# Optimization experiments

Measured on AMD Instinct MI355X. Metric: run time of the kernel, lower is better.

The kernel has to match this reference:

```python
import jax, jax.numpy as jnp
import numpy as np

EMBED_DIM = 768
NUM_HEADS = 12
HEAD_DIM = EMBED_DIM // NUM_HEADS
SEGMENT_LENGTHS = [2048, 4096, 8192]
DILATION_RATES = [1, 2, 4]
SCALE = 1.0 / np.sqrt(HEAD_DIM)
B, S = 1, 8192


def setup_inputs() -> dict:
    key = jax.random.key(0)
    ks = jax.random.split(key, 5)
    std = 1.0 / np.sqrt(EMBED_DIM)
    return {
        "x": jax.random.normal(ks[0], (B, S, EMBED_DIM), dtype=jnp.float32),
        "Wqkv": jax.random.normal(ks[1], (EMBED_DIM, 3 * EMBED_DIM), dtype=jnp.float32) * std,
        "bqkv": jax.random.normal(ks[2], (3 * EMBED_DIM,), dtype=jnp.float32) * 0.01,
        "Wout": jax.random.normal(ks[3], (EMBED_DIM, EMBED_DIM), dtype=jnp.float32) * std,
        "bout": jax.random.normal(ks[4], (EMBED_DIM,), dtype=jnp.float32) * 0.01,
    }


def _attend(q, k, v):
    # q,k,v: [B,H,L,D]; full softmax attention (non-causal)
    scores = jnp.einsum("bhqd,bhkd->bhqk", q, k) * SCALE
    w = jax.nn.softmax(scores, axis=-1)
    return jnp.einsum("bhqk,bhkd->bhqd", w, v)


def reference(x, Wqkv, bqkv, Wout, bout):
    b, s, _ = x.shape
    qkv = x @ Wqkv + bqkv                                  # [B,S,3E]
    qkv = qkv.reshape(b, s, 3, NUM_HEADS, HEAD_DIM)
    qkv = jnp.transpose(qkv, (2, 0, 3, 1, 4))              # [3,B,H,S,D]
    q, k, v = qkv[0], qkv[1], qkv[2]

    outputs = []
    for seg_len, dil in zip(SEGMENT_LENGTHS, DILATION_RATES):
        if seg_len > s:
            continue
        if dil > 1:
            idx = np.arange(0, s, dil)[:seg_len]           # static indices
            seg_out = _attend(q[:, :, idx, :], k[:, :, idx, :], v[:, :, idx, :])
            full = jnp.zeros((b, NUM_HEADS, s, HEAD_DIM), dtype=seg_out.dtype)
            full = full.at[:, :, idx, :].set(seg_out)
        else:
            seg_out = _attend(q[:, :, :seg_len, :], k[:, :, :seg_len, :], v[:, :, :seg_len, :])
            pad = s - seg_out.shape[2]
            full = jnp.pad(seg_out, ((0, 0), (0, 0), (0, pad), (0, 0))) if pad > 0 else seg_out
        outputs.append(full)

    out = jnp.mean(jnp.stack(outputs), axis=0) if len(outputs) > 1 else outputs[0]
    out = jnp.transpose(out, (0, 2, 1, 3)).reshape(b, s, EMBED_DIM)
    return out @ Wout + bout
```

## Files before the change

kernel.cpp:

```cpp
#include <hip/hip_runtime.h>
#include <hip/hip_bf16.h>

typedef float f32x4 __attribute__((ext_vector_type(4)));
typedef float fvec4 __attribute__((ext_vector_type(4)));
typedef __bf16 bf16x8 __attribute__((ext_vector_type(8)));

__device__ inline float fexp2(float x) {
#if __has_builtin(__builtin_amdgcn_exp2f)
    return __builtin_amdgcn_exp2f(x);
#else
    return exp2f(x);
#endif
}

#define MFMA_BF16(a, b, c) __builtin_amdgcn_mfma_f32_16x16x32_bf16((a), (b), (c), 0, 0, 0)

__device__ __forceinline__ void gl2lds16(const void* g, void* l) {
    __builtin_amdgcn_global_load_lds((const __attribute__((address_space(1))) void*)g,
                                     (__attribute__((address_space(3))) void*)l, 16, 0, 0);
}

#define SEG1OFF ((size_t)12 * 2048 * 64)
#define SEG2OFF ((size_t)12 * 6144 * 64)
#define QSCALE 0.18033688f

__global__ __launch_bounds__(256) void cvt_kernel(const float* __restrict__ in,
                                                  __bf16* __restrict__ out, int n8) {
    int i = blockIdx.x * 256 + threadIdx.x;
    if (i >= n8) return;
    fvec4 a = ((const fvec4*)in)[2 * i];
    fvec4 b = ((const fvec4*)in)[2 * i + 1];
    bf16x8 o;
    o[0] = (__bf16)a[0]; o[1] = (__bf16)a[1]; o[2] = (__bf16)a[2]; o[3] = (__bf16)a[3];
    o[4] = (__bf16)b[0]; o[5] = (__bf16)b[1]; o[6] = (__bf16)b[2]; o[7] = (__bf16)b[3];
    ((bf16x8*)out)[i] = o;
}

__global__ __launch_bounds__(256) void transpose_cvt_kernel(const float* __restrict__ src,
                                                            __bf16* __restrict__ dst, int N) {
    int n = blockIdx.x * 256 + threadIdx.x;
    int kg = blockIdx.y;
    if (n >= N) return;
    bf16x8 o;
#pragma unroll
    for (int j = 0; j < 8; j++) o[j] = (__bf16)src[(size_t)(kg * 8 + j) * N + n];
    *(bf16x8*)&dst[(size_t)n * 768 + kg * 8] = o;
}

__global__ __launch_bounds__(256) void vtrans_kernel(const __bf16* __restrict__ Vc,
                                                     __bf16* __restrict__ Vt) {
    __shared__ __bf16 T[64][68];
    int bid = blockIdx.x;
    int Lc, head, t;
    size_t soff;
    if (bid < 768)       { Lc = 4096; head = bid >> 6; t = bid & 63; soff = SEG1OFF; }
    else if (bid < 1152) { int i = bid - 768; Lc = 2048; head = i >> 5; t = i & 31; soff = 0; }
    else                 { int i = bid - 1152; Lc = 2048; head = i >> 5; t = i & 31; soff = SEG2OFF; }
    const __bf16* src = Vc + soff + (size_t)head * Lc * 64;
    __bf16* dst = Vt + soff + (size_t)head * 64 * Lc;
    int tid = threadIdx.x;
#pragma unroll
    for (int it = 0; it < 2; it++) {
        int s = tid + it * 256;
        int kvr = s >> 3, d8 = (s & 7) * 8;
        bf16x8 vv = *(const bf16x8*)&src[(size_t)(t * 64 + kvr) * 64 + d8];
#pragma unroll
        for (int j = 0; j < 8; j++) T[d8 + j][kvr] = vv[j];
    }
    __syncthreads();
#pragma unroll
    for (int it = 0; it < 2; it++) {
        int s = tid + it * 256;
        int d = s >> 3, ck = s & 7;
        int kb = (ck >> 2) * 32 + (ck & 3) * 4;
        bf16x8 o;
#pragma unroll
        for (int J = 0; J < 8; J++) o[J] = T[d][kb + (J & 3) + (J >> 2) * 16];
        *(bf16x8*)&dst[(size_t)d * Lc + t * 64 + ck * 8] = o;
    }
}

__global__ __launch_bounds__(256, 2) void gemm_kernel(
    const __bf16* __restrict__ Ab, const __bf16* __restrict__ Bt,
    const float* __restrict__ bias,
    __bf16* __restrict__ Qc, __bf16* __restrict__ Kc, __bf16* __restrict__ Vc,
    float* __restrict__ Co, int mode) {
    __shared__ __align__(16) char smem[34816];
    __bf16* Al = (__bf16*)smem;
    __bf16* Bl = Al + 128 * 64;
    __bf16* T  = (__bf16*)smem;
    int tid = threadIdx.x;
    int wave = tid >> 6, lane = tid & 63;
    int quad = lane >> 4, l15 = lane & 15;
    int bm = blockIdx.x * 128, bn = blockIdx.y * 128;
    int wm = (wave >> 1) * 64, wn = (wave & 1) * 64;
    int swzA = tid & 7;
    f32x4 acc[4][4] = {};
    for (int k0 = 0; k0 < 768; k0 += 64) {
        __syncthreads();
#pragma unroll
        for (int j = 0; j < 4; j++) {
            int s = j * 256 + tid;
            int row = s >> 3;
            int ch = swzA ^ (row & 7);
            gl2lds16(&Ab[(size_t)(bm + row) * 768 + k0 + ch * 8],
                     (char*)smem + j * 4096 + wave * 1024);
            gl2lds16(&Bt[(size_t)(bn + row) * 768 + k0 + ch * 8],
                     (char*)smem + 16384 + j * 4096 + wave * 1024);
        }
        __syncthreads();
#pragma unroll
        for (int ks = 0; ks < 2; ks++) {
            bf16x8 af[4], bfr[4];
#pragma unroll
            for (int i = 0; i < 4; i++) {
                int row = wm + i * 16 + l15;
                af[i] = *(const bf16x8*)&Al[row * 64 + (((ks * 4 + quad) ^ (row & 7)) * 8)];
            }
#pragma unroll
            for (int j = 0; j < 4; j++) {
                int row = wn + j * 16 + l15;
                bfr[j] = *(const bf16x8*)&Bl[row * 64 + (((ks * 4 + quad) ^ (row & 7)) * 8)];
            }
#pragma unroll
            for (int i = 0; i < 4; i++)
#pragma unroll
                for (int j = 0; j < 4; j++)
                    acc[i][j] = MFMA_BF16(af[i], bfr[j], acc[i][j]);
        }
    }
    if (mode == 0) {
        int which = blockIdx.y / 6;
        int h0 = (blockIdx.y % 6) * 2;
        float scl = which == 0 ? QSCALE : 1.0f;
        float bv[4];
#pragma unroll
        for (int j = 0; j < 4; j++) bv[j] = bias[bn + wn + j * 16 + l15];
        __syncthreads();
#pragma unroll
        for (int i = 0; i < 4; i++)
#pragma unroll
            for (int j = 0; j < 4; j++) {
                int col = wn + j * 16 + l15;
#pragma unroll
                for (int r = 0; r < 4; r++) {
                    int row = wm + i * 16 + quad * 4 + r;
                    int ch = ((col >> 3) & 8) | (((col >> 3) & 7) ^ (row & 7));
                    T[row * 136 + ch * 8 + (col & 7)] =
                        (__bf16)((acc[i][j][r] + bv[j]) * scl);
                }
            }
        __syncthreads();
        __bf16* dst = which == 0 ? Qc : (which == 1 ? Kc : Vc);
        int rr = tid >> 4;
        int c8 = tid & 15;
        int hh = c8 >> 3, d8 = c8 & 7;
        int h = h0 + hh;
        __bf16* p0 = dst + ((size_t)h * 2048 * 64) + d8 * 8;
        __bf16* p1 = dst + SEG1OFF + ((size_t)h * 4096 * 64) + d8 * 8;
        __bf16* p2 = dst + SEG2OFF + ((size_t)h * 2048 * 64) + d8 * 8;
#pragma unroll
        for (int pass = 0; pass < 8; pass++) {
            int row = pass * 16 + rr;
            int pos = bm + row;
            int ch = (c8 & 8) | ((c8 & 7) ^ (row & 7));
            bf16x8 v = *(const bf16x8*)&T[row * 136 + ch * 8];
            if (pos < 2048) *(bf16x8*)&p0[(size_t)pos * 64] = v;
            if (!(pos & 1)) *(bf16x8*)&p1[(size_t)(pos >> 1) * 64] = v;
            if (!(pos & 3)) *(bf16x8*)&p2[(size_t)(pos >> 2) * 64] = v;
        }
    } else {
        int quad4 = quad * 4;
#pragma unroll
        for (int j = 0; j < 4; j++) {
            int c = bn + wn + j * 16 + l15;
            float bv = bias[c];
#pragma unroll
            for (int i = 0; i < 4; i++)
#pragma unroll
                for (int r = 0; r < 4; r++) {
                    int row = bm + wm + i * 16 + quad4 + r;
                    Co[(size_t)row * 768 + c] = acc[i][j][r] + bv;
                }
        }
    }
}

__global__ __launch_bounds__(256, 2) void attn_kernel(
    const __bf16* __restrict__ Qcb, const __bf16* __restrict__ Kcb,
    const __bf16* __restrict__ Vtb,
    float* __restrict__ O0, float* __restrict__ O1a, float* __restrict__ O1b,
    float* __restrict__ O2, float* __restrict__ L0, float* __restrict__ L1a,
    float* __restrict__ L1b, float* __restrict__ L2) {
    __shared__ __bf16 Kl[64 * 64];
    __shared__ __bf16 Vl[64 * 64];
    int bid = blockIdx.x;
    int seg, half = 0, head, qt, Lc;
    if (bid < 768)      { int i = bid >> 1; half = bid & 1; head = i >> 5; qt = i & 31; Lc = 4096; seg = 1; }
    else if (bid < 960) { int i = bid - 768; head = i >> 4; qt = i & 15; Lc = 2048; seg = 0; }
    else                { int i = bid - 960; head = i >> 4; qt = i & 15; Lc = 2048; seg = 2; }
    size_t soff = seg == 0 ? 0 : (seg == 1 ? SEG1OFF : SEG2OFF);
    const __bf16* Qh = Qcb + soff + (size_t)head * Lc * 64;
    const __bf16* Kh = Kcb + soff + (size_t)head * Lc * 64;
    const __bf16* Vh = Vtb + soff + (size_t)head * 64 * Lc;
    float* Ob;
    float* Lb;
    if (seg == 0)      { Ob = O0; Lb = L0 + head * 2048; }
    else if (seg == 1) { Ob = half ? O1b : O1a; Lb = (half ? L1b : L1a) + head * 4096; }
    else               { Ob = O2; Lb = L2 + head * 2048; }
    int kvb = (seg == 1) ? half * 32 : 0;
    int tid = threadIdx.x, wave = tid >> 6, lane = tid & 63;
    int quad = lane >> 4, l15 = lane & 15;
    bf16x8 qf[2][2];
#pragma unroll
    for (int qg = 0; qg < 2; qg++) {
        size_t qpos = (size_t)(qt * 128 + wave * 32 + qg * 16 + l15);
        qf[qg][0] = *(const bf16x8*)&Qh[qpos * 64 + quad * 8];
        qf[qg][1] = *(const bf16x8*)&Qh[qpos * 64 + 32 + quad * 8];
    }
    f32x4 o[2][4] = {};
    float lrun[2] = {0.f, 0.f};
    int kv0 = tid >> 3, cl0 = tid & 7;
    int kdb0 = cl0 ^ (kv0 & 7);
    int kv1 = kv0 + 32, kdb1 = cl0 ^ (kv1 & 7);
    char* KlB = (char*)Kl;
    char* VlB = (char*)Vl;
    int swz = l15 & 7;
    for (int nt = 0; nt < 32; nt++) {
        int t0 = (kvb + nt) * 64;
        __syncthreads();
        gl2lds16(&Kh[(size_t)(t0 + kv0) * 64 + kdb0 * 8], KlB + wave * 1024);
        gl2lds16(&Kh[(size_t)(t0 + kv1) * 64 + kdb1 * 8], KlB + 4096 + wave * 1024);
        gl2lds16(&Vh[(size_t)kv0 * Lc + t0 + kdb0 * 8], VlB + wave * 1024);
        gl2lds16(&Vh[(size_t)kv1 * Lc + t0 + kdb1 * 8], VlB + 4096 + wave * 1024);
        __syncthreads();
        f32x4 sarr[4][2];
#pragma unroll
        for (int c = 0; c < 4; c++) {
            int krow = (c * 16 + l15) * 64;
            bf16x8 kf0 = *(const bf16x8*)&Kl[krow + ((quad ^ swz) * 8)];
            bf16x8 kf1 = *(const bf16x8*)&Kl[krow + (((4 + quad) ^ swz) * 8)];
#pragma unroll
            for (int qg = 0; qg < 2; qg++) {
                f32x4 z = {};
                z = MFMA_BF16(kf0, qf[qg][0], z);
                sarr[c][qg] = MFMA_BF16(kf1, qf[qg][1], z);
            }
        }
        bf16x8 pf8[2][2];
#pragma unroll
        for (int qg = 0; qg < 2; qg++)
#pragma unroll
            for (int c = 0; c < 4; c++)
#pragma unroll
                for (int r = 0; r < 4; r++) {
                    float p = fexp2(sarr[c][qg][r]);
                    lrun[qg] += p;
                    pf8[qg][c >> 1][(c & 1) * 4 + r] = (__bf16)p;
                }
#pragma unroll
        for (int u = 0; u < 2; u++)
#pragma unroll
            for (int ds = 0; ds < 4; ds++) {
                int d = ds * 16 + l15;
                bf16x8 vf = *(const bf16x8*)&Vl[d * 64 + (((u * 4 + quad) ^ swz) * 8)];
                o[0][ds] = MFMA_BF16(vf, pf8[0][u], o[0][ds]);
                o[1][ds] = MFMA_BF16(vf, pf8[1][u], o[1][ds]);
            }
    }
#pragma unroll
    for (int qg = 0; qg < 2; qg++) {
        float l = lrun[qg];
        l += __shfl_xor(l, 16, 64);
        l += __shfl_xor(l, 32, 64);
        int pos = qt * 128 + wave * 32 + qg * 16 + l15;
        float* orow = Ob + (size_t)pos * 768 + head * 64;
#pragma unroll
        for (int ds = 0; ds < 4; ds++)
            *(f32x4*)&orow[ds * 16 + quad * 4] = o[qg][ds];
        if (lane < 16) Lb[qt * 128 + wave * 32 + qg * 16 + lane] = l;
    }
}

__global__ __launch_bounds__(256) void combine_kernel(
    const float* __restrict__ O0, const float* __restrict__ O1a,
    const float* __restrict__ O1b, const float* __restrict__ O2,
    const float* __restrict__ L0, const float* __restrict__ L1a,
    const float* __restrict__ L1b, const float* __restrict__ L2,
    __bf16* __restrict__ attnF) {
    int g = blockIdx.x * 256 + threadIdx.x;
    int q = g / 96;
    int cs = (g - q * 96) * 8;
    int head = cs >> 6;
    f32x4 a0 = {}, a1 = {};
    if (q < 2048) {
        float inv = 1.0f / L0[head * 2048 + q];
        const f32x4* p = (const f32x4*)&O0[(size_t)q * 768 + cs];
        a0 += p[0] * inv; a1 += p[1] * inv;
    }
    if (!(q & 1)) {
        int p1 = q >> 1;
        float inv = 1.0f / (L1a[head * 4096 + p1] + L1b[head * 4096 + p1]);
        const f32x4* pa = (const f32x4*)&O1a[(size_t)p1 * 768 + cs];
        const f32x4* pb = (const f32x4*)&O1b[(size_t)p1 * 768 + cs];
        a0 += (pa[0] + pb[0]) * inv; a1 += (pa[1] + pb[1]) * inv;
    }
    if (!(q & 3)) {
        int p2 = q >> 2;
        float inv = 1.0f / L2[head * 2048 + p2];
        const f32x4* p = (const f32x4*)&O2[(size_t)p2 * 768 + cs];
        a0 += p[0] * inv; a1 += p[1] * inv;
    }
    const float third = 1.0f / 3.0f;
    bf16x8 ov;
    ov[0] = (__bf16)(a0[0] * third); ov[1] = (__bf16)(a0[1] * third);
    ov[2] = (__bf16)(a0[2] * third); ov[3] = (__bf16)(a0[3] * third);
    ov[4] = (__bf16)(a1[0] * third); ov[5] = (__bf16)(a1[1] * third);
    ov[6] = (__bf16)(a1[2] * third); ov[7] = (__bf16)(a1[3] * third);
    *(bf16x8*)&attnF[(size_t)q * 768 + cs] = ov;
}

extern "C" void kernel_launch(void* const* d_in, const int* in_sizes, int n_in,
                              void* d_out, int out_size, void* d_ws, size_t ws_size,
                              hipStream_t stream) {
    const float* x    = (const float*)d_in[0];
    const float* Wqkv = (const float*)d_in[1];
    const float* bqkv = (const float*)d_in[2];
    const float* Wout = (const float*)d_in[3];
    const float* bout = (const float*)d_in[4];
    float* out = (float*)d_out;
    (void)in_sizes; (void)n_in; (void)out_size; (void)ws_size;

    char* ws = (char*)d_ws;
    size_t off = 0;
    auto take = [&](size_t bytes) -> void* {
        void* p = ws + off;
        off += (bytes + 255) & ~(size_t)255;
        return p;
    };
    const size_t QKV_ELEMS = (size_t)12 * 8192 * 64;
    __bf16* xb    = (__bf16*)take((size_t)8192 * 768 * 2);
    __bf16* WqkvT = (__bf16*)take((size_t)2304 * 768 * 2);
    __bf16* WoutT = (__bf16*)take((size_t)768 * 768 * 2);
    __bf16* Qc    = (__bf16*)take(QKV_ELEMS * 2);
    __bf16* Kc    = (__bf16*)take(QKV_ELEMS * 2);
    __bf16* Vc    = (__bf16*)take(QKV_ELEMS * 2);
    __bf16* Vt    = (__bf16*)take(QKV_ELEMS * 2);
    float*  O0    = (float*)take((size_t)2048 * 768 * 4);
    float*  O1a   = (float*)take((size_t)4096 * 768 * 4);
    float*  O1b   = (float*)take((size_t)4096 * 768 * 4);
    float*  O2    = (float*)take((size_t)2048 * 768 * 4);
    float*  L0    = (float*)take((size_t)12 * 2048 * 4);
    float*  L1a   = (float*)take((size_t)12 * 4096 * 4);
    float*  L1b   = (float*)take((size_t)12 * 4096 * 4);
    float*  L2    = (float*)take((size_t)12 * 2048 * 4);
    __bf16* attnF = Qc;

    cvt_kernel<<<3072, 256, 0, stream>>>(x, xb, 8192 * 768 / 8);
    transpose_cvt_kernel<<<dim3(9, 96), 256, 0, stream>>>(Wqkv, WqkvT, 2304);
    transpose_cvt_kernel<<<dim3(3, 96), 256, 0, stream>>>(Wout, WoutT, 768);
    gemm_kernel<<<dim3(64, 18), 256, 0, stream>>>(xb, WqkvT, bqkv, Qc, Kc, Vc,
                                                  nullptr, 0);
    vtrans_kernel<<<1536, 256, 0, stream>>>(Vc, Vt);
    attn_kernel<<<1152, 256, 0, stream>>>(Qc, Kc, Vt, O0, O1a, O1b, O2, L0, L1a, L1b, L2);
    combine_kernel<<<3072, 256, 0, stream>>>(O0, O1a, O1b, O2, L0, L1a, L1b, L2, attnF);
    gemm_kernel<<<dim3(64, 6), 256, 0, stream>>>(attnF, WoutT, bout, nullptr, nullptr,
                                                 nullptr, out, 1);
}
```

Measured before the change: 259.7 us.

## Split long-segment attention KV into four pieces and retile output GEMM

The 4096-length segment's attention is now split four ways along the KV axis instead of two. Each block runs 16 KV tiles, the launch grows to 1920 blocks, and the combine kernel sums four partial outputs and row sums. The output projection gets its own kernel with 64-row tiles, giving 768 blocks instead of 384 so the GPU is filled better. The probability packing uses the packed bf16 convert builtin, and some partial buffers reuse dead workspace (xb, Vc). The trade-off is extra partial-output traffic and a heavier combine kernel.

```diff
diff --git a/kernel.cpp b/kernel.cpp
--- a/kernel.cpp
+++ b/kernel.cpp
@@ -4,12 +4,22 @@
 typedef float f32x4 __attribute__((ext_vector_type(4)));
 typedef float fvec4 __attribute__((ext_vector_type(4)));
 typedef __bf16 bf16x8 __attribute__((ext_vector_type(8)));
+typedef __bf16 bf16x2 __attribute__((ext_vector_type(2)));
 
 __device__ inline float fexp2(float x) {
 #if __has_builtin(__builtin_amdgcn_exp2f)
     return __builtin_amdgcn_exp2f(x);
 #else
     return exp2f(x);
+#endif
+}
+
+__device__ __forceinline__ bf16x2 pk_bf16(float a, float b) {
+#if __has_builtin(__builtin_amdgcn_cvt_pk_bf16_f32)
+    auto t = __builtin_amdgcn_cvt_pk_bf16_f32(a, b);
+    return __builtin_bit_cast(bf16x2, t);
+#else
+    bf16x2 r; r[0] = (__bf16)a; r[1] = (__bf16)b; return r;
 #endif
 }
 
@@ -80,11 +90,10 @@
     }
 }
 
-__global__ __launch_bounds__(256, 2) void gemm_kernel(
+__global__ __launch_bounds__(256, 2) void gemm_qkv_kernel(
     const __bf16* __restrict__ Ab, const __bf16* __restrict__ Bt,
     const float* __restrict__ bias,
-    __bf16* __restrict__ Qc, __bf16* __restrict__ Kc, __bf16* __restrict__ Vc,
-    float* __restrict__ Co, int mode) {
+    __bf16* __restrict__ Qc, __bf16* __restrict__ Kc, __bf16* __restrict__ Vc) {
     __shared__ __align__(16) char smem[34816];
     __bf16* Al = (__bf16*)smem;
     __bf16* Bl = Al + 128 * 64;
@@ -129,60 +138,109 @@
                     acc[i][j] = MFMA_BF16(af[i], bfr[j], acc[i][j]);
         }
     }
-    if (mode == 0) {
-        int which = blockIdx.y / 6;
-        int h0 = (blockIdx.y % 6) * 2;
-        float scl = which == 0 ? QSCALE : 1.0f;
-        float bv[4];
-#pragma unroll
-        for (int j = 0; j < 4; j++) bv[j] = bias[bn + wn + j * 16 + l15];
-        __syncthreads();
+    int which = blockIdx.y / 6;
+    int h0 = (blockIdx.y % 6) * 2;
+    float scl = which == 0 ? QSCALE : 1.0f;
+    float bv[4];
+#pragma unroll
+    for (int j = 0; j < 4; j++) bv[j] = bias[bn + wn + j * 16 + l15];
+    __syncthreads();
+#pragma unroll
+    for (int i = 0; i < 4; i++)
+#pragma unroll
+        for (int j = 0; j < 4; j++) {
+            int col = wn + j * 16 + l15;
+#pragma unroll
+            for (int r = 0; r < 4; r++) {
+                int row = wm + i * 16 + quad * 4 + r;
+                int ch = ((col >> 3) & 8) | (((col >> 3) & 7) ^ (row & 7));
+                T[row * 136 + ch * 8 + (col & 7)] =
+                    (__bf16)((acc[i][j][r] + bv[j]) * scl);
+            }
+        }
+    __syncthreads();
+    __bf16* dst = which == 0 ? Qc : (which == 1 ? Kc : Vc);
+    int rr = tid >> 4;
+    int c8 = tid & 15;
+    int hh = c8 >> 3, d8 = c8 & 7;
+    int h = h0 + hh;
+    __bf16* p0 = dst + ((size_t)h * 2048 * 64) + d8 * 8;
+    __bf16* p1 = dst + SEG1OFF + ((size_t)h * 4096 * 64) + d8 * 8;
+    __bf16* p2 = dst + SEG2OFF + ((size_t)h * 2048 * 64) + d8 * 8;
+#pragma unroll
+    for (int pass = 0; pass < 8; pass++) {
+        int row = pass * 16 + rr;
+        int pos = bm + row;
+        int ch = (c8 & 8) | ((c8 & 7) ^ (row & 7));
+        bf16x8 v = *(const bf16x8*)&T[row * 136 + ch * 8];
+        if (pos < 2048) *(bf16x8*)&p0[(size_t)pos * 64] = v;
+        if (!(pos & 1)) *(bf16x8*)&p1[(size_t)(pos >> 1) * 64] = v;
+        if (!(pos & 3)) *(bf16x8*)&p2[(size_t)(pos >> 2) * 64] = v;
+    }
+}
+
+__global__ __launch_bounds__(256) void gemm_out_kernel(
+    const __bf16* __restrict__ Ab, const __bf16* __restrict__ Bt,
+    const float* __restrict__ bias, float* __restrict__ Co) {
+    __shared__ __align__(16) char smem[24576];
+    __bf16* Al = (__bf16*)smem;
+    __bf16* Bl = Al + 64 * 64;
+    int tid = threadIdx.x;
+    int wave = tid >> 6, lane = tid & 63;
+    int quad = lane >> 4, l15 = lane & 15;
+    int bm = blockIdx.x * 64, bn = blockIdx.y * 128;
+    int wn = wave * 32;
+    f32x4 acc[4][2] = {};
+    for (int k0 = 0; k0 < 768; k0 += 64) {
+        __syncthreads();
+#pragma unroll
+        for (int j = 0; j < 2; j++) {
+            int s = j * 256 + tid;
+            int row = s >> 3;
+            int ch = (s & 7) ^ (row & 7);
+            gl2lds16(&Ab[(size_t)(bm + row) * 768 + k0 + ch * 8],
+                     (char*)smem + j * 4096 + wave * 1024);
+        }
+#pragma unroll
+        for (int j = 0; j < 4; j++) {
+            int s = j * 256 + tid;
+            int row = s >> 3;
+            int ch = (s & 7) ^ (row & 7);
+            gl2lds16(&Bt[(size_t)(bn + row) * 768 + k0 + ch * 8],
+                     (char*)smem + 8192 + j * 4096 + wave * 1024);
+        }
+        __syncthreads();
+#pragma unroll
+        for (int ks = 0; ks < 2; ks++) {
+            bf16x8 af[4], bfr[2];
+#pragma unroll
+            for (int i = 0; i < 4; i++) {
+                int row = i * 16 + l15;
+                af[i] = *(const bf16x8*)&Al[row * 64 + (((ks * 4 + quad) ^ (row & 7)) * 8)];
+            }
+#pragma unroll
+            for (int j = 0; j < 2; j++) {
+                int row = wn + j * 16 + l15;
+                bfr[j] = *(const bf16x8*)&Bl[row * 64 + (((ks * 4 + quad) ^ (row & 7)) * 8)];
+            }
+#pragma unroll
+            for (int i = 0; i < 4; i++)
+#pragma unroll
+                for (int j = 0; j < 2; j++)
+                    acc[i][j] = MFMA_BF16(af[i], bfr[j], acc[i][j]);
+        }
+    }
+#pragma unroll
+    for (int j = 0; j < 2; j++) {
+        int c = bn + wn + j * 16 + l15;
+        float bv = bias[c];
 #pragma unroll
         for (int i = 0; i < 4; i++)
 #pragma unroll
-            for (int j = 0; j < 4; j++) {
-                int col = wn + j * 16 + l15;
-#pragma unroll
-                for (int r = 0; r < 4; r++) {
-                    int row = wm + i * 16 + quad * 4 + r;
-                    int ch = ((col >> 3) & 8) | (((col >> 3) & 7) ^ (row & 7));
-                    T[row * 136 + ch * 8 + (col & 7)] =
-                        (__bf16)((acc[i][j][r] + bv[j]) * scl);
-                }
-            }
-        __syncthreads();
-        __bf16* dst = which == 0 ? Qc : (which == 1 ? Kc : Vc);
-        int rr = tid >> 4;
-        int c8 = tid & 15;
-        int hh = c8 >> 3, d8 = c8 & 7;
-        int h = h0 + hh;
-        __bf16* p0 = dst + ((size_t)h * 2048 * 64) + d8 * 8;
-        __bf16* p1 = dst + SEG1OFF + ((size_t)h * 4096 * 64) + d8 * 8;
-        __bf16* p2 = dst + SEG2OFF + ((size_t)h * 2048 * 64) + d8 * 8;
-#pragma unroll
-        for (int pass = 0; pass < 8; pass++) {
-            int row = pass * 16 + rr;
-            int pos = bm + row;
-            int ch = (c8 & 8) | ((c8 & 7) ^ (row & 7));
-            bf16x8 v = *(const bf16x8*)&T[row * 136 + ch * 8];
-            if (pos < 2048) *(bf16x8*)&p0[(size_t)pos * 64] = v;
-            if (!(pos & 1)) *(bf16x8*)&p1[(size_t)(pos >> 1) * 64] = v;
-            if (!(pos & 3)) *(bf16x8*)&p2[(size_t)(pos >> 2) * 64] = v;
-        }
-    } else {
-        int quad4 = quad * 4;
-#pragma unroll
-        for (int j = 0; j < 4; j++) {
-            int c = bn + wn + j * 16 + l15;
-            float bv = bias[c];
-#pragma unroll
-            for (int i = 0; i < 4; i++)
-#pragma unroll
-                for (int r = 0; r < 4; r++) {
-                    int row = bm + wm + i * 16 + quad4 + r;
-                    Co[(size_t)row * 768 + c] = acc[i][j][r] + bv;
-                }
-        }
+            for (int r = 0; r < 4; r++) {
+                int row = bm + i * 16 + quad * 4 + r;
+                Co[(size_t)row * 768 + c] = acc[i][j][r] + bv;
+            }
     }
 }
 
@@ -190,15 +248,17 @@
     const __bf16* __restrict__ Qcb, const __bf16* __restrict__ Kcb,
     const __bf16* __restrict__ Vtb,
     float* __restrict__ O0, float* __restrict__ O1a, float* __restrict__ O1b,
-    float* __restrict__ O2, float* __restrict__ L0, float* __restrict__ L1a,
-    float* __restrict__ L1b, float* __restrict__ L2) {
+    float* __restrict__ O1c, float* __restrict__ O1d, float* __restrict__ O2,
+    float* __restrict__ L0, float* __restrict__ L1a, float* __restrict__ L1b,
+    float* __restrict__ L1c, float* __restrict__ L1d, float* __restrict__ L2) {
     __shared__ __bf16 Kl[64 * 64];
     __shared__ __bf16 Vl[64 * 64];
     int bid = blockIdx.x;
-    int seg, half = 0, head, qt, Lc;
-    if (bid < 768)      { int i = bid >> 1; half = bid & 1; head = i >> 5; qt = i & 31; Lc = 4096; seg = 1; }
-    else if (bid < 960) { int i = bid - 768; head = i >> 4; qt = i & 15; Lc = 2048; seg = 0; }
-    else                { int i = bid - 960; head = i >> 4; qt = i & 15; Lc = 2048; seg = 2; }
+    int seg, piece = 0, head, qt, Lc, iters;
+    if (bid < 192)      { seg = 0; head = bid >> 4; qt = bid & 15; Lc = 2048; iters = 32; }
+    else if (bid < 384) { int i = bid - 192; seg = 2; head = i >> 4; qt = i & 15; Lc = 2048; iters = 32; }
+    else                { int i = bid - 384; seg = 1; head = i >> 7; int r = i & 127;
+                          qt = r >> 2; piece = r & 3; Lc = 4096; iters = 16; }
     size_t soff = seg == 0 ? 0 : (seg == 1 ? SEG1OFF : SEG2OFF);
     const __bf16* Qh = Qcb + soff + (size_t)head * Lc * 64;
     const __bf16* Kh = Kcb + soff + (size_t)head * Lc * 64;
@@ -206,9 +266,12 @@
     float* Ob;
     float* Lb;
     if (seg == 0)      { Ob = O0; Lb = L0 + head * 2048; }
-    else if (seg == 1) { Ob = half ? O1b : O1a; Lb = (half ? L1b : L1a) + head * 4096; }
-    else               { Ob = O2; Lb = L2 + head * 2048; }
-    int kvb = (seg == 1) ? half * 32 : 0;
+    else if (seg == 2) { Ob = O2; Lb = L2 + head * 2048; }
+    else {
+        Ob = piece == 0 ? O1a : (piece == 1 ? O1b : (piece == 2 ? O1c : O1d));
+        Lb = (piece == 0 ? L1a : (piece == 1 ? L1b : (piece == 2 ? L1c : L1d))) + head * 4096;
+    }
+    int kvb = piece * 16;
     int tid = threadIdx.x, wave = tid >> 6, lane = tid & 63;
     int quad = lane >> 4, l15 = lane & 15;
     bf16x8 qf[2][2];
@@ -226,7 +289,7 @@
     char* KlB = (char*)Kl;
     char* VlB = (char*)Vl;
     int swz = l15 & 7;
-    for (int nt = 0; nt < 32; nt++) {
+    for (int nt = 0; nt < iters; nt++) {
         int t0 = (kvb + nt) * 64;
         __syncthreads();
         gl2lds16(&Kh[(size_t)(t0 + kv0) * 64 + kdb0 * 8], KlB + wave * 1024);
@@ -247,25 +310,27 @@
                 sarr[c][qg] = MFMA_BF16(kf1, qf[qg][1], z);
             }
         }
-        bf16x8 pf8[2][2];
+        union { bf16x8 v8; bf16x2 v2[4]; } pf8[2][2];
 #pragma unroll
         for (int qg = 0; qg < 2; qg++)
 #pragma unroll
-            for (int c = 0; c < 4; c++)
-#pragma unroll
-                for (int r = 0; r < 4; r++) {
-                    float p = fexp2(sarr[c][qg][r]);
-                    lrun[qg] += p;
-                    pf8[qg][c >> 1][(c & 1) * 4 + r] = (__bf16)p;
-                }
+            for (int c = 0; c < 4; c++) {
+                float p0 = fexp2(sarr[c][qg][0]);
+                float p1 = fexp2(sarr[c][qg][1]);
+                float p2 = fexp2(sarr[c][qg][2]);
+                float p3 = fexp2(sarr[c][qg][3]);
+                lrun[qg] += (p0 + p1) + (p2 + p3);
+                pf8[qg][c >> 1].v2[(c & 1) * 2 + 0] = pk_bf16(p0, p1);
+                pf8[qg][c >> 1].v2[(c & 1) * 2 + 1] = pk_bf16(p2, p3);
+            }
 #pragma unroll
         for (int u = 0; u < 2; u++)
 #pragma unroll
             for (int ds = 0; ds < 4; ds++) {
                 int d = ds * 16 + l15;
                 bf16x8 vf = *(const bf16x8*)&Vl[d * 64 + (((u * 4 + quad) ^ swz) * 8)];
-                o[0][ds] = MFMA_BF16(vf, pf8[0][u], o[0][ds]);
-                o[1][ds] = MFMA_BF16(vf, pf8[1][u], o[1][ds]);
+                o[0][ds] = MFMA_BF16(vf, pf8[0][u].v8, o[0][ds]);
+                o[1][ds] = MFMA_BF16(vf, pf8[1][u].v8, o[1][ds]);
             }
     }
 #pragma unroll
@@ -284,9 +349,11 @@
 
 __global__ __launch_bounds__(256) void combine_kernel(
     const float* __restrict__ O0, const float* __restrict__ O1a,
-    const float* __restrict__ O1b, const float* __restrict__ O2,
+    const float* __restrict__ O1b, const float* __restrict__ O1c,
+    const float* __restrict__ O1d, const float* __restrict__ O2,
     const float* __restrict__ L0, const float* __restrict__ L1a,
-    const float* __restrict__ L1b, const float* __restrict__ L2,
+    const float* __restrict__ L1b, const float* __restrict__ L1c,
+    const float* __restrict__ L1d, const float* __restrict__ L2,
     __bf16* __restrict__ attnF) {
     int g = blockIdx.x * 256 + threadIdx.x;
     int q = g / 96;
@@ -300,10 +367,15 @@
     }
     if (!(q & 1)) {
         int p1 = q >> 1;
-        float inv = 1.0f / (L1a[head * 4096 + p1] + L1b[head * 4096 + p1]);
-        const f32x4* pa = (const f32x4*)&O1a[(size_t)p1 * 768 + cs];
-        const f32x4* pb = (const f32x4*)&O1b[(size_t)p1 * 768 + cs];
-        a0 += (pa[0] + pb[0]) * inv; a1 += (pa[1] + pb[1]) * inv;
+        int li = head * 4096 + p1;
+        float inv = 1.0f / (L1a[li] + L1b[li] + L1c[li] + L1d[li]);
+        size_t ro = (size_t)p1 * 768 + cs;
+        const f32x4* pa = (const f32x4*)&O1a[ro];
+        const f32x4* pb = (const f32x4*)&O1b[ro];
+        const f32x4* pc = (const f32x4*)&O1c[ro];
+        const f32x4* pd = (const f32x4*)&O1d[ro];
+        a0 += ((pa[0] + pb[0]) + (pc[0] + pd[0])) * inv;
+        a1 += ((pa[1] + pb[1]) + (pc[1] + pd[1])) * inv;
     }
     if (!(q & 3)) {
         int p2 = q >> 2;
@@ -346,24 +418,28 @@
     __bf16* Kc    = (__bf16*)take(QKV_ELEMS * 2);
     __bf16* Vc    = (__bf16*)take(QKV_ELEMS * 2);
     __bf16* Vt    = (__bf16*)take(QKV_ELEMS * 2);
-    float*  O0    = (float*)take((size_t)2048 * 768 * 4);
     float*  O1a   = (float*)take((size_t)4096 * 768 * 4);
     float*  O1b   = (float*)take((size_t)4096 * 768 * 4);
-    float*  O2    = (float*)take((size_t)2048 * 768 * 4);
+    float*  O1c   = (float*)take((size_t)4096 * 768 * 4);
     float*  L0    = (float*)take((size_t)12 * 2048 * 4);
     float*  L1a   = (float*)take((size_t)12 * 4096 * 4);
     float*  L1b   = (float*)take((size_t)12 * 4096 * 4);
+    float*  L1c   = (float*)take((size_t)12 * 4096 * 4);
+    float*  L1d   = (float*)take((size_t)12 * 4096 * 4);
     float*  L2    = (float*)take((size_t)12 * 2048 * 4);
+    float*  O0    = (float*)xb;
+    float*  O2    = O0 + (size_t)2048 * 768;
+    float*  O1d   = (float*)Vc;
     __bf16* attnF = Qc;
 
     cvt_kernel<<<3072, 256, 0, stream>>>(x, xb, 8192 * 768 / 8);
     transpose_cvt_kernel<<<dim3(9, 96), 256, 0, stream>>>(Wqkv, WqkvT, 2304);
     transpose_cvt_kernel<<<dim3(3, 96), 256, 0, stream>>>(Wout, WoutT, 768);
-    gemm_kernel<<<dim3(64, 18), 256, 0, stream>>>(xb, WqkvT, bqkv, Qc, Kc, Vc,
-                                                  nullptr, 0);
+    gemm_qkv_kernel<<<dim3(64, 18), 256, 0, stream>>>(xb, WqkvT, bqkv, Qc, Kc, Vc);
     vtrans_kernel<<<1536, 256, 0, stream>>>(Vc, Vt);
-    attn_kernel<<<1152, 256, 0, stream>>>(Qc, Kc, Vt, O0, O1a, O1b, O2, L0, L1a, L1b, L2);
-    combine_kernel<<<3072, 256, 0, stream>>>(O0, O1a, O1b, O2, L0, L1a, L1b, L2, attnF);
-    gemm_kernel<<<dim3(64, 6), 256, 0, stream>>>(attnF, WoutT, bout, nullptr, nullptr,
-                                                 nullptr, out, 1);
-}
+    attn_kernel<<<1920, 256, 0, stream>>>(Qc, Kc, Vt, O0, O1a, O1b, O1c, O1d, O2,
+                                          L0, L1a, L1b, L1c, L1d, L2);
+    combine_kernel<<<3072, 256, 0, stream>>>(O0, O1a, O1b, O1c, O1d, O2,
+                                             L0, L1a, L1b, L1c, L1d, L2, attnF);
+    gemm_out_kernel<<<dim3(128, 6), 256, 0, stream>>>(attnF, WoutT, bout, out);
+}
```

Result: no change. 254.9 us (-1.8%).
